# Kernel tuning notes

Measured on AMD Instinct MI355X. Metric: run time of the kernel, lower is better.

Reference implementation:

```python
import jax, jax.numpy as jnp
import jax.lax as lax
import numpy as np

B, T, I, HS = 32, 2048, 256, 256
H = HS // 2  # per-direction hidden (hidden_size even -> fwd/bwd both H)


def setup_inputs() -> dict:
    key = jax.random.key(0)
    ks = jax.random.split(key, 10)
    s = 1.0 / np.sqrt(H)
    u = lambda k, shape: jax.random.uniform(k, shape, jnp.float32, -s, s)
    x = jax.random.normal(ks[0], (B, T, I), jnp.float32)
    lengths = jax.random.randint(ks[1], (B,), 1, T + 1)
    return {
        "x": x,
        "lengths": lengths,
        "Wf_ih": u(ks[2], (4 * H, I)), "Wf_hh": u(ks[3], (4 * H, H)),
        "bf_ih": u(ks[4], (4 * H,)), "bf_hh": u(ks[5], (4 * H,)),
        "Wb_ih": u(ks[6], (4 * H, I)), "Wb_hh": u(ks[7], (4 * H, H)),
        "bb_ih": u(ks[8], (4 * H,)), "bb_hh": u(ks[9], (4 * H,)),
    }


def _lstm_scan(x_seq, W_ih, W_hh, b_ih, b_hh):
    # x_seq: [B, T, I] -> hidden states per step [B, T, H]
    xg = jnp.einsum('bti,gi->btg', x_seq, W_ih) + b_ih  # input gates precomputed

    def step(carry, xg_t):
        h, c = carry
        gates = xg_t + h @ W_hh.T + b_hh  # [B, 4H]
        i, f, g, o = jnp.split(gates, 4, axis=-1)
        c = jax.nn.sigmoid(f) * c + jax.nn.sigmoid(i) * jnp.tanh(g)
        h = jax.nn.sigmoid(o) * jnp.tanh(c)
        return (h, c), h

    b, hdim = x_seq.shape[0], W_hh.shape[1]
    init = (jnp.zeros((b, hdim), x_seq.dtype), jnp.zeros((b, hdim), x_seq.dtype))
    _, hs = lax.scan(step, init, jnp.swapaxes(xg, 0, 1))  # [T, B, H]
    return jnp.swapaxes(hs, 0, 1)


def _flip_padded_seq(x, lengths):
    # reverse the first `length` steps of each sequence, keep padding in place
    t = jnp.arange(x.shape[1])[None, :]
    L = lengths[:, None]
    idx = jnp.where(t < L, L - 1 - t, t)  # [B, T]
    return jnp.take_along_axis(x, idx[:, :, None], axis=1)


def reference(x, lengths, Wf_ih, Wf_hh, bf_ih, bf_hh, Wb_ih, Wb_hh, bb_ih, bb_hh):
    fwd = _lstm_scan(x, Wf_ih, Wf_hh, bf_ih, bf_hh)
    x_rev = _flip_padded_seq(x, lengths)
    bwd = _lstm_scan(x_rev, Wb_ih, Wb_hh, bb_ih, bb_hh)
    return jnp.concatenate([fwd, bwd], axis=-1)  # [B, T, hidden_size]
```

## Files before the change

kernel.cpp:

```cpp
#include <hip/hip_runtime.h>
#include <hip/hip_fp16.h>

#define B_  32
#define T_  2048
#define I_  256
#define H_  128

typedef _Float16 f16;
typedef _Float16 f16x2 __attribute__((ext_vector_type(2)));
typedef _Float16 f16x4 __attribute__((ext_vector_type(4)));
typedef _Float16 f16x8 __attribute__((ext_vector_type(8)));
typedef float    f32x4 __attribute__((ext_vector_type(4)));

#if __has_builtin(__builtin_amdgcn_fdot2)
#define FDOT2(a, b, c) __builtin_amdgcn_fdot2((a), (b), (c), false)
#else
static __device__ __forceinline__ float FDOT2(f16x2 a, f16x2 b, float c) {
  return c + (float)a[0] * (float)b[0] + (float)a[1] * (float)b[1];
}
#endif

static __device__ __forceinline__ f16x2 asf16x2(unsigned u) {
  return __builtin_bit_cast(f16x2, u);
}

static __device__ __forceinline__ float fast_sig(float x) {
  float e = __builtin_amdgcn_exp2f(-1.44269504089f * x);
  return __builtin_amdgcn_rcpf(1.0f + e);
}
static __device__ __forceinline__ float fast_tanh(float x) {
  float e = __builtin_amdgcn_exp2f(-2.88539008178f * x);
  return 2.0f * __builtin_amdgcn_rcpf(1.0f + e) - 1.0f;
}

#define BARRIER_LDS()                                   \
  __builtin_amdgcn_sched_barrier(0);                    \
  asm volatile("s_waitcnt lgkmcnt(0)" ::: "memory");    \
  __builtin_amdgcn_s_barrier();                         \
  __builtin_amdgcn_sched_barrier(0)

__global__ __launch_bounds__(256) void xg_gemm(
    const float* __restrict__ x,
    const float* __restrict__ Wf, const float* __restrict__ Wb,
    const float* __restrict__ bf_ih, const float* __restrict__ bf_hh,
    const float* __restrict__ bb_ih, const float* __restrict__ bb_hh,
    f16* __restrict__ xg)
{
  __shared__ f16 xs[128][136];
  __shared__ f16 wt[128][136];

  const int tid = threadIdx.x;
  const int m0  = blockIdx.y * 128;
  const int n0  = blockIdx.x * 128;

  const float* Wsrc; const float* bih; const float* bhh; int nb;
  if (n0 < 512) { Wsrc = Wf; bih = bf_ih; bhh = bf_hh; nb = n0; }
  else          { Wsrc = Wb; bih = bb_ih; bhh = bb_hh; nb = n0 - 512; }

  const int w  = tid >> 6;
  const int l  = tid & 63;
  const int lr = l & 15;
  const int lk = (l >> 4) * 8;

  f32x4 acc[2][8] = {};

  #pragma unroll
  for (int kh = 0; kh < 2; ++kh) {
    #pragma unroll
    for (int it = 0; it < 16; ++it) {
      int idx = it * 256 + tid;
      int row = idx >> 5, c4 = idx & 31;
      float4 v = *(const float4*)&x[(size_t)(m0 + row) * I_ + kh * 128 + c4 * 4];
      f16x4 h4 = { (f16)v.x, (f16)v.y, (f16)v.z, (f16)v.w };
      *(f16x4*)&xs[row][c4 * 4] = h4;
    }
    #pragma unroll
    for (int it = 0; it < 16; ++it) {
      int idx = it * 256 + tid;
      int row = idx >> 5, c4 = idx & 31;
      float4 v = *(const float4*)&Wsrc[(size_t)(nb + row) * I_ + kh * 128 + c4 * 4];
      f16x4 h4 = { (f16)v.x, (f16)v.y, (f16)v.z, (f16)v.w };
      *(f16x4*)&wt[row][c4 * 4] = h4;
    }
    __syncthreads();

    #pragma unroll
    for (int ks = 0; ks < 4; ++ks) {
      int kk = ks * 32 + lk;
      f16x8 a0 = *(const f16x8*)&xs[w * 32 + lr][kk];
      f16x8 a1 = *(const f16x8*)&xs[w * 32 + 16 + lr][kk];
      #pragma unroll
      for (int nt = 0; nt < 8; ++nt) {
        f16x8 bf = *(const f16x8*)&wt[nt * 16 + lr][kk];
        acc[0][nt] = __builtin_amdgcn_mfma_f32_16x16x32_f16(a0, bf, acc[0][nt], 0, 0, 0);
        acc[1][nt] = __builtin_amdgcn_mfma_f32_16x16x32_f16(a1, bf, acc[1][nt], 0, 0, 0);
      }
    }
    __syncthreads();
  }

  #pragma unroll
  for (int mt = 0; mt < 2; ++mt) {
    #pragma unroll
    for (int nt = 0; nt < 8; ++nt) {
      int nloc = nt * 16 + lr;
      float bias = bih[nb + nloc] + bhh[nb + nloc];
      #pragma unroll
      for (int r = 0; r < 4; ++r) {
        int m = m0 + w * 32 + mt * 16 + (l >> 4) * 4 + r;
        xg[(size_t)m * 1024 + n0 + nloc] = (f16)(acc[mt][nt][r] + bias);
      }
    }
  }
}

__global__ __launch_bounds__(256, 1) void birnn_rec(
    const f16* __restrict__ xg,
    const float* __restrict__ Wfhh, const float* __restrict__ Wbhh,
    const int* __restrict__ lengths,
    float* __restrict__ out)
{
  const int tid = threadIdx.x;
  const int dir = blockIdx.x >> 5;
  const int b   = blockIdx.x & 31;
  const float* Whh = dir ? Wbhh : Wfhh;
  const int g0 = tid, g1 = tid + 256;
  const int L  = lengths[b];

  unsigned w0[64], w1[64];
  #pragma unroll
  for (int j = 0; j < 32; ++j) {
    float4 v = *(const float4*)&Whh[(size_t)g0 * H_ + j * 4];
    w0[2 * j]     = __builtin_bit_cast(unsigned, (f16x2){ (f16)v.x, (f16)v.y });
    w0[2 * j + 1] = __builtin_bit_cast(unsigned, (f16x2){ (f16)v.z, (f16)v.w });
    float4 u = *(const float4*)&Whh[(size_t)g1 * H_ + j * 4];
    w1[2 * j]     = __builtin_bit_cast(unsigned, (f16x2){ (f16)u.x, (f16)u.y });
    w1[2 * j + 1] = __builtin_bit_cast(unsigned, (f16x2){ (f16)u.z, (f16)u.w });
  }

  __shared__ __align__(16) unsigned hbuf[2][64];
  __shared__ float gx[256];

  if (tid < 64) { hbuf[0][tid] = 0u; }
  float c = 0.0f;
  __syncthreads();

  auto rowof = [&](int t) -> size_t {
    int it = t;
    if (dir) it = (t < L) ? (L - 1 - t) : t;
    return ((size_t)(b * T_ + it)) * 1024 + (size_t)dir * 512;
  };

  f16 pa0, pa1, pb0, pb1;
  { size_t r = rowof(0); pa0 = xg[r + g0]; pa1 = xg[r + g1]; }
  { size_t r = rowof(1); pb0 = xg[r + g0]; pb1 = xg[r + g1]; }

#define STEP(t, P0, P1, HR, HW)                                              \
  {                                                                          \
    float xg0 = (float)(P0);                                                 \
    float xg1 = (float)(P1);                                                 \
    if ((t) + 2 < T_) {                                                      \
      size_t r2 = rowof((t) + 2);                                            \
      (P0) = xg[r2 + g0];                                                    \
      (P1) = xg[r2 + g1];                                                    \
    }                                                                        \
    float aA[4] = { xg0, 0.f, 0.f, 0.f };                                    \
    float aB[4] = { xg1, 0.f, 0.f, 0.f };                                    \
    _Pragma("unroll")                                                        \
    for (int j4 = 0; j4 < 16; ++j4) {                                        \
      uint4 hv = *(const uint4*)&(HR)[j4 * 4];                               \
      aA[0] = FDOT2(asf16x2(hv.x), asf16x2(w0[j4 * 4 + 0]), aA[0]);          \
      aB[0] = FDOT2(asf16x2(hv.x), asf16x2(w1[j4 * 4 + 0]), aB[0]);          \
      aA[1] = FDOT2(asf16x2(hv.y), asf16x2(w0[j4 * 4 + 1]), aA[1]);          \
      aB[1] = FDOT2(asf16x2(hv.y), asf16x2(w1[j4 * 4 + 1]), aB[1]);          \
      aA[2] = FDOT2(asf16x2(hv.z), asf16x2(w0[j4 * 4 + 2]), aA[2]);          \
      aB[2] = FDOT2(asf16x2(hv.z), asf16x2(w1[j4 * 4 + 2]), aB[2]);          \
      aA[3] = FDOT2(asf16x2(hv.w), asf16x2(w0[j4 * 4 + 3]), aA[3]);          \
      aB[3] = FDOT2(asf16x2(hv.w), asf16x2(w1[j4 * 4 + 3]), aB[3]);          \
    }                                                                        \
    float sumA = (aA[0] + aA[1]) + (aA[2] + aA[3]);                          \
    float sumB = (aB[0] + aB[1]) + (aB[2] + aB[3]);                          \
    float s0, s1;                                                            \
    if (tid >= 128) {                   \
      s0 = fast_sig(sumA);                                       \
      s1 = fast_sig(sumB);                                       \
      gx[tid - 128] = s0;                                                    \
      gx[tid]       = s1;                                                    \
    } else {                                                                 \
      s0 = fast_sig(sumA);                                       \
      s1 = fast_tanh(sumB);                                     \
    }                                                                        \
    BARRIER_LDS();                                                           \
    if (tid < 128) {                                                         \
      float fs = gx[tid];                                                    \
      float os = gx[128 + tid];                                              \
      c = fs * c + s0 * s1;                                                  \
      float hval = os * fast_tanh(c);                                        \
      ((unsigned short*)(HW))[tid] =                                         \
          __builtin_bit_cast(unsigned short, (f16)hval);                     \
      out[((size_t)(b * T_ + (t))) * 256 + dir * 128 + tid] = hval;          \
    }                                                                        \
    BARRIER_LDS();                                                           \
  }

  for (int tt = 0; tt < T_; tt += 2) {
    STEP(tt,     pa0, pa1, hbuf[0], hbuf[1]);
    STEP(tt + 1, pb0, pb1, hbuf[1], hbuf[0]);
  }
#undef STEP
}

extern "C" void kernel_launch(void* const* d_in, const int* in_sizes, int n_in,
                              void* d_out, int out_size, void* d_ws, size_t ws_size,
                              hipStream_t stream) {
  const float* x      = (const float*)d_in[0];
  const int*   lengths= (const int*)  d_in[1];
  const float* Wf_ih  = (const float*)d_in[2];
  const float* Wf_hh  = (const float*)d_in[3];
  const float* bf_ih  = (const float*)d_in[4];
  const float* bf_hh  = (const float*)d_in[5];
  const float* Wb_ih  = (const float*)d_in[6];
  const float* Wb_hh  = (const float*)d_in[7];
  const float* bb_ih  = (const float*)d_in[8];
  const float* bb_hh  = (const float*)d_in[9];
  float* out = (float*)d_out;
  f16*   xg  = (f16*)d_ws;

  (void)in_sizes; (void)n_in; (void)out_size; (void)ws_size;

  xg_gemm<<<dim3(8, 512), 256, 0, stream>>>(x, Wf_ih, Wb_ih,
                                            bf_ih, bf_hh, bb_ih, bb_hh, xg);
  birnn_rec<<<dim3(64), 256, 0, stream>>>(xg, Wf_hh, Wb_hh, lengths, out);
}
```

Measured before the change: 1.352 ms.

## Use MFMA for recurrent matvec with 512-thread blocks and single barrier per step

Replaces the per-thread fdot2 recurrent matvec with 16x16x32 f16 MFMA instructions. Only row 0 of the A tile is real and holds h; the other rows are wasted. Each block now uses 8 waves, and each wave owns 16 hidden units across all four gates. That lets one lane compute every gate for its unit, so the gx LDS exchange and one of the two barriers per step go away. The cost is 16-row MFMA padding overhead and MFMA latency on the serial critical path, in exchange for fewer instructions and less synchronisation per step.

Result: slower. 1.599 ms (+18.2%).

```diff
diff --git a/kernel.cpp b/kernel.cpp
--- a/kernel.cpp
+++ b/kernel.cpp
@@ -7,22 +7,9 @@
 #define H_  128
 
 typedef _Float16 f16;
-typedef _Float16 f16x2 __attribute__((ext_vector_type(2)));
 typedef _Float16 f16x4 __attribute__((ext_vector_type(4)));
 typedef _Float16 f16x8 __attribute__((ext_vector_type(8)));
 typedef float    f32x4 __attribute__((ext_vector_type(4)));
-
-#if __has_builtin(__builtin_amdgcn_fdot2)
-#define FDOT2(a, b, c) __builtin_amdgcn_fdot2((a), (b), (c), false)
-#else
-static __device__ __forceinline__ float FDOT2(f16x2 a, f16x2 b, float c) {
-  return c + (float)a[0] * (float)b[0] + (float)a[1] * (float)b[1];
-}
-#endif
-
-static __device__ __forceinline__ f16x2 asf16x2(unsigned u) {
-  return __builtin_bit_cast(f16x2, u);
-}
 
 static __device__ __forceinline__ float fast_sig(float x) {
   float e = __builtin_amdgcn_exp2f(-1.44269504089f * x);
@@ -114,35 +101,39 @@
   }
 }
 
-__global__ __launch_bounds__(256, 1) void birnn_rec(
+__global__ __launch_bounds__(512, 1) void birnn_rec(
     const f16* __restrict__ xg,
     const float* __restrict__ Wfhh, const float* __restrict__ Wbhh,
     const int* __restrict__ lengths,
     float* __restrict__ out)
 {
-  const int tid = threadIdx.x;
-  const int dir = blockIdx.x >> 5;
-  const int b   = blockIdx.x & 31;
+  const int tid  = threadIdx.x;
+  const int wave = tid >> 6;
+  const int l    = tid & 63;
+  const int c    = l & 15;
+  const int kgrp = l >> 4;
+  const int dir  = blockIdx.x >> 5;
+  const int b    = blockIdx.x & 31;
   const float* Whh = dir ? Wbhh : Wfhh;
-  const int g0 = tid, g1 = tid + 256;
-  const int L  = lengths[b];
-
-  unsigned w0[64], w1[64];
+  const int L    = lengths[b];
+
+  f16x8 bfrag[4][4];
   #pragma unroll
-  for (int j = 0; j < 32; ++j) {
-    float4 v = *(const float4*)&Whh[(size_t)g0 * H_ + j * 4];
-    w0[2 * j]     = __builtin_bit_cast(unsigned, (f16x2){ (f16)v.x, (f16)v.y });
-    w0[2 * j + 1] = __builtin_bit_cast(unsigned, (f16x2){ (f16)v.z, (f16)v.w });
-    float4 u = *(const float4*)&Whh[(size_t)g1 * H_ + j * 4];
-    w1[2 * j]     = __builtin_bit_cast(unsigned, (f16x2){ (f16)u.x, (f16)u.y });
-    w1[2 * j + 1] = __builtin_bit_cast(unsigned, (f16x2){ (f16)u.z, (f16)u.w });
-  }
-
-  __shared__ __align__(16) unsigned hbuf[2][64];
-  __shared__ float gx[256];
-
-  if (tid < 64) { hbuf[0][tid] = 0u; }
-  float c = 0.0f;
+  for (int q = 0; q < 4; ++q) {
+    int n = q * 128 + wave * 16 + c;
+    #pragma unroll
+    for (int ks = 0; ks < 4; ++ks) {
+      int k0 = ks * 32 + kgrp * 8;
+      float4 va = *(const float4*)&Whh[(size_t)n * H_ + k0];
+      float4 vb = *(const float4*)&Whh[(size_t)n * H_ + k0 + 4];
+      bfrag[q][ks] = (f16x8){ (f16)va.x, (f16)va.y, (f16)va.z, (f16)va.w,
+                              (f16)vb.x, (f16)vb.y, (f16)vb.z, (f16)vb.w };
+    }
+  }
+
+  __shared__ __align__(16) f16 hbuf[2][128];
+  if (tid < 128) hbuf[0][tid] = (f16)0.0f;
+  float cstate = 0.0f;
   __syncthreads();
 
   auto rowof = [&](int t) -> size_t {
@@ -150,62 +141,70 @@
     if (dir) it = (t < L) ? (L - 1 - t) : t;
     return ((size_t)(b * T_ + it)) * 1024 + (size_t)dir * 512;
   };
-
-  f16 pa0, pa1, pb0, pb1;
-  { size_t r = rowof(0); pa0 = xg[r + g0]; pa1 = xg[r + g1]; }
-  { size_t r = rowof(1); pb0 = xg[r + g0]; pb1 = xg[r + g1]; }
-
-#define STEP(t, P0, P1, HR, HW)                                              \
-  {                                                                          \
-    float xg0 = (float)(P0);                                                 \
-    float xg1 = (float)(P1);                                                 \
-    if ((t) + 2 < T_) {                                                      \
-      size_t r2 = rowof((t) + 2);                                            \
-      (P0) = xg[r2 + g0];                                                    \
-      (P1) = xg[r2 + g1];                                                    \
-    }                                                                        \
-    float aA[4] = { xg0, 0.f, 0.f, 0.f };                                    \
-    float aB[4] = { xg1, 0.f, 0.f, 0.f };                                    \
-    _Pragma("unroll")                                                        \
-    for (int j4 = 0; j4 < 16; ++j4) {                                        \
-      uint4 hv = *(const uint4*)&(HR)[j4 * 4];                               \
-      aA[0] = FDOT2(asf16x2(hv.x), asf16x2(w0[j4 * 4 + 0]), aA[0]);          \
-      aB[0] = FDOT2(asf16x2(hv.x), asf16x2(w1[j4 * 4 + 0]), aB[0]);          \
-      aA[1] = FDOT2(asf16x2(hv.y), asf16x2(w0[j4 * 4 + 1]), aA[1]);          \
-      aB[1] = FDOT2(asf16x2(hv.y), asf16x2(w1[j4 * 4 + 1]), aB[1]);          \
-      aA[2] = FDOT2(asf16x2(hv.z), asf16x2(w0[j4 * 4 + 2]), aA[2]);          \
-      aB[2] = FDOT2(asf16x2(hv.z), asf16x2(w1[j4 * 4 + 2]), aB[2]);          \
-      aA[3] = FDOT2(asf16x2(hv.w), asf16x2(w0[j4 * 4 + 3]), aA[3]);          \
-      aB[3] = FDOT2(asf16x2(hv.w), asf16x2(w1[j4 * 4 + 3]), aB[3]);          \
-    }                                                                        \
-    float sumA = (aA[0] + aA[1]) + (aA[2] + aA[3]);                          \
-    float sumB = (aB[0] + aB[1]) + (aB[2] + aB[3]);                          \
-    float s0, s1;                                                            \
-    if (tid >= 128) {                   \
-      s0 = fast_sig(sumA);                                       \
-      s1 = fast_sig(sumB);                                       \
-      gx[tid - 128] = s0;                                                    \
-      gx[tid]       = s1;                                                    \
-    } else {                                                                 \
-      s0 = fast_sig(sumA);                                       \
-      s1 = fast_tanh(sumB);                                     \
-    }                                                                        \
-    BARRIER_LDS();                                                           \
-    if (tid < 128) {                                                         \
-      float fs = gx[tid];                                                    \
-      float os = gx[128 + tid];                                              \
-      c = fs * c + s0 * s1;                                                  \
-      float hval = os * fast_tanh(c);                                        \
-      ((unsigned short*)(HW))[tid] =                                         \
-          __builtin_bit_cast(unsigned short, (f16)hval);                     \
-      out[((size_t)(b * T_ + (t))) * 256 + dir * 128 + tid] = hval;          \
-    }                                                                        \
-    BARRIER_LDS();                                                           \
+  const int goff = wave * 16 + c;
+
+  f16 pa[4], pb[4];
+  {
+    size_t r0 = rowof(0), r1 = rowof(1);
+    #pragma unroll
+    for (int q = 0; q < 4; ++q) {
+      pa[q] = xg[r0 + q * 128 + goff];
+      pb[q] = xg[r1 + q * 128 + goff];
+    }
+  }
+
+  const bool row0 = (l < 16);
+
+#define STEP(t, P, HR, HW)                                                    \
+  {                                                                           \
+    f32x4 a0 = {}, a1 = {}, a2 = {}, a3 = {};                                 \
+    a0[0] = row0 ? (float)P[0] : 0.0f;                                        \
+    a1[0] = row0 ? (float)P[1] : 0.0f;                                        \
+    a2[0] = row0 ? (float)P[2] : 0.0f;                                        \
+    a3[0] = row0 ? (float)P[3] : 0.0f;                                        \
+    if ((t) + 2 < T_) {                                                       \
+      size_t r2 = rowof((t) + 2);                                             \
+      P[0] = xg[r2 + 0 * 128 + goff];                                         \
+      P[1] = xg[r2 + 1 * 128 + goff];                                         \
+      P[2] = xg[r2 + 2 * 128 + goff];                                         \
+      P[3] = xg[r2 + 3 * 128 + goff];                                         \
+    }                                                                         \
+    f16x8 af0 = *(const f16x8*)&(HR)[kgrp * 8];                               \
+    f16x8 af1 = *(const f16x8*)&(HR)[32 + kgrp * 8];                          \
+    f16x8 af2 = *(const f16x8*)&(HR)[64 + kgrp * 8];                          \
+    f16x8 af3 = *(const f16x8*)&(HR)[96 + kgrp * 8];                          \
+    a0 = __builtin_amdgcn_mfma_f32_16x16x32_f16(af0, bfrag[0][0], a0, 0, 0, 0); \
+    a1 = __builtin_amdgcn_mfma_f32_16x16x32_f16(af0, bfrag[1][0], a1, 0, 0, 0); \
+    a2 = __builtin_amdgcn_mfma_f32_16x16x32_f16(af0, bfrag[2][0], a2, 0, 0, 0); \
+    a3 = __builtin_amdgcn_mfma_f32_16x16x32_f16(af0, bfrag[3][0], a3, 0, 0, 0); \
+    a0 = __builtin_amdgcn_mfma_f32_16x16x32_f16(af1, bfrag[0][1], a0, 0, 0, 0); \
+    a1 = __builtin_amdgcn_mfma_f32_16x16x32_f16(af1, bfrag[1][1], a1, 0, 0, 0); \
+    a2 = __builtin_amdgcn_mfma_f32_16x16x32_f16(af1, bfrag[2][1], a2, 0, 0, 0); \
+    a3 = __builtin_amdgcn_mfma_f32_16x16x32_f16(af1, bfrag[3][1], a3, 0, 0, 0); \
+    a0 = __builtin_amdgcn_mfma_f32_16x16x32_f16(af2, bfrag[0][2], a0, 0, 0, 0); \
+    a1 = __builtin_amdgcn_mfma_f32_16x16x32_f16(af2, bfrag[1][2], a1, 0, 0, 0); \
+    a2 = __builtin_amdgcn_mfma_f32_16x16x32_f16(af2, bfrag[2][2], a2, 0, 0, 0); \
+    a3 = __builtin_amdgcn_mfma_f32_16x16x32_f16(af2, bfrag[3][2], a3, 0, 0, 0); \
+    a0 = __builtin_amdgcn_mfma_f32_16x16x32_f16(af3, bfrag[0][3], a0, 0, 0, 0); \
+    a1 = __builtin_amdgcn_mfma_f32_16x16x32_f16(af3, bfrag[1][3], a1, 0, 0, 0); \
+    a2 = __builtin_amdgcn_mfma_f32_16x16x32_f16(af3, bfrag[2][3], a2, 0, 0, 0); \
+    a3 = __builtin_amdgcn_mfma_f32_16x16x32_f16(af3, bfrag[3][3], a3, 0, 0, 0); \
+    if (row0) {                                                               \
+      float is = fast_sig(a0[0]);                                             \
+      float fs = fast_sig(a1[0]);                                             \
+      float gt = fast_tanh(a2[0]);                                            \
+      float os = fast_sig(a3[0]);                                             \
+      cstate = fs * cstate + is * gt;                                         \
+      float hval = os * fast_tanh(cstate);                                    \
+      (HW)[goff] = (f16)hval;                                                 \
+      out[((size_t)(b * T_ + (t))) * 256 + dir * 128 + goff] = hval;          \
+    }                                                                         \
+    BARRIER_LDS();                                                            \
   }
 
   for (int tt = 0; tt < T_; tt += 2) {
-    STEP(tt,     pa0, pa1, hbuf[0], hbuf[1]);
-    STEP(tt + 1, pb0, pb1, hbuf[1], hbuf[0]);
+    STEP(tt,     pa, hbuf[0], hbuf[1]);
+    STEP(tt + 1, pb, hbuf[1], hbuf[0]);
   }
 #undef STEP
 }
@@ -230,5 +229,5 @@
 
   xg_gemm<<<dim3(8, 512), 256, 0, stream>>>(x, Wf_ih, Wb_ih,
                                             bf_ih, bf_hh, bb_ih, bb_hh, xg);
-  birnn_rec<<<dim3(64), 256, 0, stream>>>(xg, Wf_hh, Wb_hh, lengths, out);
-}
+  birnn_rec<<<dim3(64), 512, 0, stream>>>(xg, Wf_hh, Wb_hh, lengths, out);
+}
```

## Pair gate rows across wave halves and exchange via shuffle, dropping one barrier

Applied to the files above, without the earlier changes.

Each hidden unit's i/g rows and f/o rows are now assigned to lanes 32 apart in the same wavefront. The partner gate activations are exchanged with a cross-lane shuffle instead of being staged through LDS. This removes the gx shared buffer and one of the two block barriers per timestep, which shortens the serial recurrence critical path. tanh is computed branch-free as a scaled sigmoid, and the h write is split across all four waves, with half the lanes computing redundantly.

New measurement: 1.347 ms. Within noise of the previous version (-0.4%).

```diff
diff --git a/kernel.cpp b/kernel.cpp
--- a/kernel.cpp
+++ b/kernel.cpp
@@ -38,6 +38,8 @@
   asm volatile("s_waitcnt lgkmcnt(0)" ::: "memory");    \
   __builtin_amdgcn_s_barrier();                         \
   __builtin_amdgcn_sched_barrier(0)
+
+#define MFMA16(a, b, c) __builtin_amdgcn_mfma_f32_16x16x32_f16((a), (b), (c), 0, 0, 0)
 
 __global__ __launch_bounds__(256) void xg_gemm(
     const float* __restrict__ x,
@@ -92,8 +94,8 @@
       #pragma unroll
       for (int nt = 0; nt < 8; ++nt) {
         f16x8 bf = *(const f16x8*)&wt[nt * 16 + lr][kk];
-        acc[0][nt] = __builtin_amdgcn_mfma_f32_16x16x32_f16(a0, bf, acc[0][nt], 0, 0, 0);
-        acc[1][nt] = __builtin_amdgcn_mfma_f32_16x16x32_f16(a1, bf, acc[1][nt], 0, 0, 0);
+        acc[0][nt] = MFMA16(a0, bf, acc[0][nt]);
+        acc[1][nt] = MFMA16(a1, bf, acc[1][nt]);
       }
     }
     __syncthreads();
@@ -120,28 +122,32 @@
     const int* __restrict__ lengths,
     float* __restrict__ out)
 {
-  const int tid = threadIdx.x;
-  const int dir = blockIdx.x >> 5;
-  const int b   = blockIdx.x & 31;
+  const int tid  = threadIdx.x;
+  const int w    = tid >> 6;
+  const int l    = tid & 63;
+  const int role = l >> 5;
+  const int ul   = w * 32 + (l & 31);
+  const int dir  = blockIdx.x >> 5;
+  const int b    = blockIdx.x & 31;
   const float* Whh = dir ? Wbhh : Wfhh;
-  const int g0 = tid, g1 = tid + 256;
-  const int L  = lengths[b];
+  const int L    = lengths[b];
+
+  const int rowA = role ? (128 + ul) : ul;
+  const int rowB = rowA + 256;
 
   unsigned w0[64], w1[64];
   #pragma unroll
   for (int j = 0; j < 32; ++j) {
-    float4 v = *(const float4*)&Whh[(size_t)g0 * H_ + j * 4];
+    float4 v = *(const float4*)&Whh[(size_t)rowA * H_ + j * 4];
     w0[2 * j]     = __builtin_bit_cast(unsigned, (f16x2){ (f16)v.x, (f16)v.y });
     w0[2 * j + 1] = __builtin_bit_cast(unsigned, (f16x2){ (f16)v.z, (f16)v.w });
-    float4 u = *(const float4*)&Whh[(size_t)g1 * H_ + j * 4];
+    float4 u = *(const float4*)&Whh[(size_t)rowB * H_ + j * 4];
     w1[2 * j]     = __builtin_bit_cast(unsigned, (f16x2){ (f16)u.x, (f16)u.y });
     w1[2 * j + 1] = __builtin_bit_cast(unsigned, (f16x2){ (f16)u.z, (f16)u.w });
   }
 
-  __shared__ __align__(16) unsigned hbuf[2][64];
-  __shared__ float gx[256];
-
-  if (tid < 64) { hbuf[0][tid] = 0u; }
+  __shared__ __align__(16) f16 hbuf[2][128];
+  if (tid < 128) hbuf[0][tid] = (f16)0.0f;
   float c = 0.0f;
   __syncthreads();
 
@@ -152,23 +158,25 @@
   };
 
   f16 pa0, pa1, pb0, pb1;
-  { size_t r = rowof(0); pa0 = xg[r + g0]; pa1 = xg[r + g1]; }
-  { size_t r = rowof(1); pb0 = xg[r + g0]; pb1 = xg[r + g1]; }
-
-#define STEP(t, P0, P1, HR, HW)                                              \
+  { size_t r = rowof(0); pa0 = xg[r + rowA]; pa1 = xg[r + rowB]; }
+  { size_t r = rowof(1); pb0 = xg[r + rowA]; pb1 = xg[r + rowB]; }
+
+  const float bscale = role ? 1.0f : 2.0f;
+  const float bmul   = role ? 1.0f : 2.0f;
+  const float badd   = role ? 0.0f : -1.0f;
+
+#define STEP(t, P0, P1, RB, WB)                                              \
   {                                                                          \
-    float xg0 = (float)(P0);                                                 \
-    float xg1 = (float)(P1);                                                 \
+    float aA[4] = { (float)(P0), 0.f, 0.f, 0.f };                            \
+    float aB[4] = { (float)(P1), 0.f, 0.f, 0.f };                            \
     if ((t) + 2 < T_) {                                                      \
       size_t r2 = rowof((t) + 2);                                            \
-      (P0) = xg[r2 + g0];                                                    \
-      (P1) = xg[r2 + g1];                                                    \
+      (P0) = xg[r2 + rowA];                                                  \
+      (P1) = xg[r2 + rowB];                                                  \
     }                                                                        \
-    float aA[4] = { xg0, 0.f, 0.f, 0.f };                                    \
-    float aB[4] = { xg1, 0.f, 0.f, 0.f };                                    \
     _Pragma("unroll")                                                        \
     for (int j4 = 0; j4 < 16; ++j4) {                                        \
-      uint4 hv = *(const uint4*)&(HR)[j4 * 4];                               \
+      uint4 hv = *(const uint4*)&hbuf[RB][j4 * 8];                           \
       aA[0] = FDOT2(asf16x2(hv.x), asf16x2(w0[j4 * 4 + 0]), aA[0]);          \
       aB[0] = FDOT2(asf16x2(hv.x), asf16x2(w1[j4 * 4 + 0]), aB[0]);          \
       aA[1] = FDOT2(asf16x2(hv.y), asf16x2(w0[j4 * 4 + 1]), aA[1]);          \
@@ -180,32 +188,27 @@
     }                                                                        \
     float sumA = (aA[0] + aA[1]) + (aA[2] + aA[3]);                          \
     float sumB = (aB[0] + aB[1]) + (aB[2] + aB[3]);                          \
-    float s0, s1;                                                            \
-    if (tid >= 128) {                   \
-      s0 = fast_sig(sumA);                                       \
-      s1 = fast_sig(sumB);                                       \
-      gx[tid - 128] = s0;                                                    \
-      gx[tid]       = s1;                                                    \
-    } else {                                                                 \
-      s0 = fast_sig(sumA);                                       \
-      s1 = fast_tanh(sumB);                                     \
+      \
+    float sA = fast_sig(sumA);                                               \
+    float sB = fast_sig(bscale * sumB) * bmul + badd;                        \
+    float pA = __shfl_xor(sA, 32, 64);                                       \
+    float pB = __shfl_xor(sB, 32, 64);                                       \
+    float is_ = role ? pA : sA;                                              \
+    float gt_ = role ? pB : sB;                                              \
+    float fs_ = role ? sA : pA;                                              \
+    float os_ = role ? sB : pB;                                              \
+    c = fs_ * c + is_ * gt_;                                                 \
+    float hval = os_ * fast_tanh(c);                                         \
+    if (!role) {                                                             \
+      hbuf[WB][ul] = (f16)hval;                                              \
+      out[((size_t)(b * T_ + (t))) * 256 + dir * 128 + ul] = hval;           \
     }                                                                        \
     BARRIER_LDS();                                                           \
-    if (tid < 128) {                                                         \
-      float fs = gx[tid];                                                    \
-      float os = gx[128 + tid];                                              \
-      c = fs * c + s0 * s1;                                                  \
-      float hval = os * fast_tanh(c);                                        \
-      ((unsigned short*)(HW))[tid] =                                         \
-          __builtin_bit_cast(unsigned short, (f16)hval);                     \
-      out[((size_t)(b * T_ + (t))) * 256 + dir * 128 + tid] = hval;          \
-    }                                                                        \
-    BARRIER_LDS();                                                           \
   }
 
   for (int tt = 0; tt < T_; tt += 2) {
-    STEP(tt,     pa0, pa1, hbuf[0], hbuf[1]);
-    STEP(tt + 1, pb0, pb1, hbuf[1], hbuf[0]);
+    STEP(tt,     pa0, pa1, 0, 1);
+    STEP(tt + 1, pb0, pb1, 1, 0);
   }
 #undef STEP
 }
```
